# Optimization experiments

Hardware: AMD Instinct MI355X
Metric: run time of the kernel (lower is better)

The kernel has to match this reference:

```python
import jax, jax.numpy as jnp
import numpy as np

COLUMN_COUNT = 1024
CELLS_PER_COLUMN = 8
NUM_CELLS = COLUMN_COUNT * CELLS_PER_COLUMN  # 8192
ACTIVATION_THRESHOLD = 13.0
PERM_CONNECTED = 0.5
PERM_INC = 0.1
PERM_DEC = 0.1


def setup_inputs() -> dict:
    key = jax.random.key(0)
    k1, k2, k3, k4 = jax.random.split(key, 4)
    active_columns = (jax.random.uniform(k1, (COLUMN_COUNT,)) < 0.02).astype(jnp.float32)
    # dense permanence matrix in [0,1); ~half connected at threshold 0.5
    segment_weights = jax.random.uniform(k2, (NUM_CELLS, NUM_CELLS), dtype=jnp.float32)
    # sparse binary previous predictive / active cell states
    predictive_cells = (jax.random.uniform(k3, (NUM_CELLS,)) < 0.01).astype(jnp.float32)
    prev_active_cells = (jax.random.uniform(k4, (NUM_CELLS,)) < 0.01).astype(jnp.float32)
    return {
        "active_columns": active_columns,
        "segment_weights": segment_weights,
        "predictive_cells": predictive_cells,
        "prev_active_cells": prev_active_cells,
    }


def reference(active_columns, segment_weights, predictive_cells, prev_active_cells):
    # --- compute_activity (vectorized over columns; no python loop) ---
    col_pred = predictive_cells.reshape(COLUMN_COUNT, CELLS_PER_COLUMN)
    col_has_pred = col_pred.sum(axis=1) > 0                      # [C] bool
    active_mask = active_columns > 0                             # [C] bool
    # per active column: use its predictions if any, else burst (all ones)
    per_col = jnp.where(col_has_pred[:, None], col_pred, 1.0)    # [C, cells]
    new_active = (per_col * active_mask[:, None].astype(col_pred.dtype)).reshape(NUM_CELLS)

    connected = (segment_weights >= PERM_CONNECTED).astype(segment_weights.dtype)
    presyn = connected @ new_active                              # [N] dense matvec
    new_predictive = (presyn >= ACTIVATION_THRESHOLD).astype(segment_weights.dtype)

    # --- anomaly: fraction of active columns that were NOT predicted ---
    num_active = jnp.sum(active_mask)
    num_predicted = jnp.sum(active_mask & col_has_pred)
    anomaly = 1.0 - num_predicted.astype(jnp.float32) / jnp.maximum(num_active, 1).astype(jnp.float32)

    # --- learn: outer-product permanence update, skipped if no prev activity ---
    delta = PERM_INC * new_active[None, :] * prev_active_cells[:, None]          # [N,N]
    decay = (PERM_DEC * 0.1) * (1.0 - new_active[None, :]) * prev_active_cells[:, None]
    updated = jnp.clip(segment_weights + delta - decay, 0.0, 1.0)
    new_segment_weights = jnp.where(prev_active_cells.sum() > 0, updated, segment_weights)

    return (new_active, new_predictive, anomaly, new_segment_weights)
```

## Files before the change

kernel.cpp:

```cpp
#include <hip/hip_runtime.h>

#define NUM_CELLS 8192
#define COLS 1024

typedef float vf4 __attribute__((ext_vector_type(4)));
typedef vf4 uvf4 __attribute__((aligned(4)));

__global__ __launch_bounds__(1024) void prep_kernel(
    const float* __restrict__ act_cols, const float* __restrict__ pred,
    float* __restrict__ out) {
  const int t = threadIdx.x;
  const vf4* __restrict__ pred4 = (const vf4*)pred;

  const vf4 p0 = pred4[t * 2 + 0];
  const vf4 p1 = pred4[t * 2 + 1];

  const float colsum = p0.x + p0.y + p0.z + p0.w + p1.x + p1.y + p1.z + p1.w;
  const bool has_pred = colsum > 0.f;
  const bool active = act_cols[t] > 0.f;

  vf4 o0, o1;
  if (active) {
    if (has_pred) { o0 = p0; o1 = p1; }
    else          { o0 = (vf4){1.f,1.f,1.f,1.f}; o1 = (vf4){1.f,1.f,1.f,1.f}; }
  } else {
    o0 = (vf4){0.f,0.f,0.f,0.f}; o1 = o0;
  }
  ((vf4*)out)[t * 2 + 0] = o0;
  ((vf4*)out)[t * 2 + 1] = o1;

  float nA = active ? 1.f : 0.f;
  float nP = (active && has_pred) ? 1.f : 0.f;

#pragma unroll
  for (int off = 32; off; off >>= 1) {
    nA += __shfl_down(nA, off);
    nP += __shfl_down(nP, off);
  }
  __shared__ float sA[16], sP[16];
  const int wid = t >> 6;
  if ((t & 63) == 0) { sA[wid] = nA; sP[wid] = nP; }
  __syncthreads();
  if (t == 0) {
    float a = 0.f, pp = 0.f;
    for (int i = 0; i < 16; i++) { a += sA[i]; pp += sP[i]; }
    out[2 * NUM_CELLS] = 1.0f - pp / fmaxf(a, 1.0f);
  }
}

__device__ __forceinline__ float upd1(float w, float a, bool learn) {
  return learn ? fminf(fmaxf(w + ((a > 0.5f) ? 0.1f : -0.01f), 0.f), 1.f) : w;
}

__global__ __launch_bounds__(256) void fused_kernel(
    const float* __restrict__ W, const float* __restrict__ prev,
    float* __restrict__ out) {
  const int lane = threadIdx.x & 63;
  const int row = (blockIdx.x << 2) | (threadIdx.x >> 6);

  const bool learn = prev[row] > 0.f;
  const float* __restrict__ Wrow = W + (size_t)row * NUM_CELLS;
  const float* __restrict__ A = out;
  float* __restrict__ Orow = out + 2 * NUM_CELLS + 1 + (size_t)row * NUM_CELLS;

  float sum = 0.f;

  if (lane == 0) {
    const vf4 w = *(const vf4*)Wrow;
    const vf4 a = *(const vf4*)A;
    sum += ((w.x >= 0.5f) ? a.x : 0.f) + ((w.y >= 0.5f) ? a.y : 0.f) +
           ((w.z >= 0.5f) ? a.z : 0.f);
    Orow[0] = upd1(w.x, a.x, learn);
    Orow[1] = upd1(w.y, a.y, learn);
    Orow[2] = upd1(w.z, a.z, learn);
    const float wl = Wrow[NUM_CELLS - 1];
    const float al = A[NUM_CELLS - 1];
    sum += (wl >= 0.5f) ? al : 0.f;
    Orow[NUM_CELLS - 1] = upd1(wl, al, learn);
  } else {
    const int j = 4 * lane - 1;
    const uvf4 w = *(const uvf4*)(Wrow + j);
    const uvf4 a = *(const uvf4*)(A + j);
    sum += ((w.x >= 0.5f) ? a.x : 0.f) + ((w.y >= 0.5f) ? a.y : 0.f) +
           ((w.z >= 0.5f) ? a.z : 0.f) + ((w.w >= 0.5f) ? a.w : 0.f);
    vf4 u;
    u.x = upd1(w.x, a.x, learn);
    u.y = upd1(w.y, a.y, learn);
    u.z = upd1(w.z, a.z, learn);
    u.w = upd1(w.w, a.w, learn);
    *(vf4*)(Orow + j) = u;
  }

  int j = 4 * (64 | lane) - 1;
  uvf4 w = *(const uvf4*)(Wrow + j);
  uvf4 a = *(const uvf4*)(A + j);
  for (int k = 1; k < 31; k++) {
    const int jn = 4 * (((k + 1) << 6) | lane) - 1;
    const uvf4 wn = *(const uvf4*)(Wrow + jn);
    const uvf4 an = *(const uvf4*)(A + jn);
    sum += ((w.x >= 0.5f) ? a.x : 0.f) + ((w.y >= 0.5f) ? a.y : 0.f) +
           ((w.z >= 0.5f) ? a.z : 0.f) + ((w.w >= 0.5f) ? a.w : 0.f);
    vf4 u;
    u.x = upd1(w.x, a.x, learn);
    u.y = upd1(w.y, a.y, learn);
    u.z = upd1(w.z, a.z, learn);
    u.w = upd1(w.w, a.w, learn);
    *(vf4*)(Orow + j) = u;
    w = wn; a = an; j = jn;
  }
  {
    sum += ((w.x >= 0.5f) ? a.x : 0.f) + ((w.y >= 0.5f) ? a.y : 0.f) +
           ((w.z >= 0.5f) ? a.z : 0.f) + ((w.w >= 0.5f) ? a.w : 0.f);
    vf4 u;
    u.x = upd1(w.x, a.x, learn);
    u.y = upd1(w.y, a.y, learn);
    u.z = upd1(w.z, a.z, learn);
    u.w = upd1(w.w, a.w, learn);
    *(vf4*)(Orow + j) = u;
  }

#pragma unroll
  for (int off = 32; off; off >>= 1) sum += __shfl_down(sum, off);
  if (lane == 0)
    out[NUM_CELLS + row] = (sum >= 13.0f) ? 1.f : 0.f;
}

extern "C" void kernel_launch(void* const* d_in, const int* in_sizes, int n_in,
                              void* d_out, int out_size, void* d_ws, size_t ws_size,
                              hipStream_t stream) {
  const float* act_cols = (const float*)d_in[0];
  const float* W = (const float*)d_in[1];
  const float* pred = (const float*)d_in[2];
  const float* prev = (const float*)d_in[3];
  float* out = (float*)d_out;
  (void)d_ws; (void)ws_size;

  prep_kernel<<<1, 1024, 0, stream>>>(act_cols, pred, out);
  fused_kernel<<<NUM_CELLS / 4, 256, 0, stream>>>(W, prev, out);
}
```

Baseline: 450.4 us.

## Assign one row per 256-thread block with fully unrolled loads

```diff
diff --git a/kernel.cpp b/kernel.cpp
--- a/kernel.cpp
+++ b/kernel.cpp
@@ -55,8 +55,8 @@
 __global__ __launch_bounds__(256) void fused_kernel(
     const float* __restrict__ W, const float* __restrict__ prev,
     float* __restrict__ out) {
-  const int lane = threadIdx.x & 63;
-  const int row = (blockIdx.x << 2) | (threadIdx.x >> 6);
+  const int t = threadIdx.x;
+  const int row = blockIdx.x;
 
   const bool learn = prev[row] > 0.f;
   const float* __restrict__ Wrow = W + (size_t)row * NUM_CELLS;
@@ -65,7 +65,7 @@
 
   float sum = 0.f;
 
-  if (lane == 0) {
+  if (t == 0) {
     const vf4 w = *(const vf4*)Wrow;
     const vf4 a = *(const vf4*)A;
     sum += ((w.x >= 0.5f) ? a.x : 0.f) + ((w.y >= 0.5f) ? a.y : 0.f) +
@@ -78,7 +78,7 @@
     sum += (wl >= 0.5f) ? al : 0.f;
     Orow[NUM_CELLS - 1] = upd1(wl, al, learn);
   } else {
-    const int j = 4 * lane - 1;
+    const int j = 4 * t - 1;
     const uvf4 w = *(const uvf4*)(Wrow + j);
     const uvf4 a = *(const uvf4*)(A + j);
     sum += ((w.x >= 0.5f) ? a.x : 0.f) + ((w.y >= 0.5f) ? a.y : 0.f) +
@@ -91,24 +91,11 @@
     *(vf4*)(Orow + j) = u;
   }
 
-  int j = 4 * (64 | lane) - 1;
-  uvf4 w = *(const uvf4*)(Wrow + j);
-  uvf4 a = *(const uvf4*)(A + j);
-  for (int k = 1; k < 31; k++) {
-    const int jn = 4 * (((k + 1) << 6) | lane) - 1;
-    const uvf4 wn = *(const uvf4*)(Wrow + jn);
-    const uvf4 an = *(const uvf4*)(A + jn);
-    sum += ((w.x >= 0.5f) ? a.x : 0.f) + ((w.y >= 0.5f) ? a.y : 0.f) +
-           ((w.z >= 0.5f) ? a.z : 0.f) + ((w.w >= 0.5f) ? a.w : 0.f);
-    vf4 u;
-    u.x = upd1(w.x, a.x, learn);
-    u.y = upd1(w.y, a.y, learn);
-    u.z = upd1(w.z, a.z, learn);
-    u.w = upd1(w.w, a.w, learn);
-    *(vf4*)(Orow + j) = u;
-    w = wn; a = an; j = jn;
-  }
-  {
+#pragma unroll
+  for (int k = 1; k < 8; k++) {
+    const int j = 4 * (k * 256 + t) - 1;
+    const uvf4 w = *(const uvf4*)(Wrow + j);
+    const uvf4 a = *(const uvf4*)(A + j);
     sum += ((w.x >= 0.5f) ? a.x : 0.f) + ((w.y >= 0.5f) ? a.y : 0.f) +
            ((w.z >= 0.5f) ? a.z : 0.f) + ((w.w >= 0.5f) ? a.w : 0.f);
     vf4 u;
@@ -121,8 +108,13 @@
 
 #pragma unroll
   for (int off = 32; off; off >>= 1) sum += __shfl_down(sum, off);
-  if (lane == 0)
-    out[NUM_CELLS + row] = (sum >= 13.0f) ? 1.f : 0.f;
+  __shared__ float s[4];
+  if ((t & 63) == 0) s[t >> 6] = sum;
+  __syncthreads();
+  if (t == 0) {
+    const float tot = s[0] + s[1] + s[2] + s[3];
+    out[NUM_CELLS + row] = (tot >= 13.0f) ? 1.f : 0.f;
+  }
 }
 
 extern "C" void kernel_launch(void* const* d_in, const int* in_sizes, int n_in,
@@ -136,5 +128,5 @@
   (void)d_ws; (void)ws_size;
 
   prep_kernel<<<1, 1024, 0, stream>>>(act_cols, pred, out);
-  fused_kernel<<<NUM_CELLS / 4, 256, 0, stream>>>(W, prev, out);
+  fused_kernel<<<NUM_CELLS, 256, 0, stream>>>(W, prev, out);
 }
```

Measured after the change: 439.8 us. 2.3% less time.
